# Kernel tuning notes

Hardware: AMD Instinct MI355X
Metric: run time of the kernel (lower is better)

## Reference

```python
import jax, jax.numpy as jnp
import numpy as np

B = 2048          # number of graphs in the batch
ACT_DIM = 14      # nodes per graph (act_dim)
C = 128           # in_channels
H = 256           # hidden_size


def _pair_edges(n):
    ii, jj = np.meshgrid(np.arange(n), np.arange(n), indexing='ij')
    m = ii != jj
    return np.stack([ii[m], jj[m]], axis=1)  # [n*(n-1), 2]


def setup_inputs() -> dict:
    key = jax.random.key(0)
    ks = jax.random.split(key, 12)
    edges_np = _pair_edges(ACT_DIM)                       # [182, 2]
    offs = (np.arange(B) * ACT_DIM)[:, None, None]
    batched = (edges_np[None] + offs).reshape(-1, 2)      # [B*182, 2]
    edge_index = jnp.asarray(batched.T, dtype=jnp.int64 if jax.config.jax_enable_x64 else jnp.int32)
    edges = jnp.asarray(edges_np, dtype=jnp.int32)

    def lin(k, o, i):
        return jax.random.normal(k, (o, i), jnp.float32) * (1.0 / np.sqrt(i))

    return {
        'state': jax.random.normal(ks[0], (B * ACT_DIM, C), jnp.float32),
        'conv_w': lin(ks[1], C, C),
        'conv_b': jnp.zeros((C,), jnp.float32),
        'lin1_w': lin(ks[2], H, 2 * C),
        'lin1_b': jax.random.normal(ks[3], (H,), jnp.float32) * 0.01,
        'lin2_w': lin(ks[4], H, H),
        'lin2_b': jax.random.normal(ks[5], (H,), jnp.float32) * 0.01,
        'mu_w': lin(ks[6], 1, H),
        'mu_b': jnp.zeros((1,), jnp.float32),
        'sig_w': lin(ks[7], 1, H),
        'sig_b': jnp.zeros((1,), jnp.float32),
        'noise': jax.random.normal(ks[8], (B, edges_np.shape[0]), jnp.float32),
        'edge_index': edge_index,
        'edges': edges,
    }


def _gcn_conv(x, edge_index, w, b):
    # Standard GCNConv: add self-loops, symmetric normalization, x @ W^T, scatter-add, + bias.
    n = x.shape[0]
    loops = jnp.arange(n, dtype=edge_index.dtype)
    src = jnp.concatenate([edge_index[0], loops])
    dst = jnp.concatenate([edge_index[1], loops])
    deg = jax.ops.segment_sum(jnp.ones_like(src, dtype=x.dtype), dst, num_segments=n)
    dinv = jax.lax.rsqrt(deg)  # deg >= 1 because of self-loops
    norm = dinv[src] * dinv[dst]                       # [E+N]
    xw = x @ w.T                                       # [N, C]
    msg = xw[src] * norm[:, None]                      # gather + scale
    return jax.ops.segment_sum(msg, dst, num_segments=n) + b


def reference(state, conv_w, conv_b, lin1_w, lin1_b, lin2_w, lin2_b,
              mu_w, mu_b, sig_w, sig_b, noise, edge_index, edges):
    out = jax.nn.relu(_gcn_conv(state, edge_index, conv_w, conv_b))
    x = (out + state).reshape(-1, ACT_DIM, C)          # [B, 14, C]
    es, ed = edges[:, 0], edges[:, 1]
    ef = jnp.concatenate([x[:, es, :], x[:, ed, :]], axis=2)   # [B, E, 2C]
    h = jax.nn.leaky_relu(jnp.einsum('bec,hc->beh', ef, lin1_w) + lin1_b)
    h = jax.nn.leaky_relu(jnp.einsum('beh,gh->beg', h, lin2_w) + lin2_b)
    mu = jax.nn.softplus(jnp.einsum('beh,oh->beo', h, mu_w) + mu_b)[..., 0]   # [B, E]
    std = jax.nn.softplus(jnp.einsum('beh,oh->beo', h, sig_w) + sig_b)[..., 0]
    action = mu + std * noise                          # Normal rsample with fixed eps
    log_prob = jnp.sum(
        -0.5 * ((action - mu) / std) ** 2 - jnp.log(std) - 0.5 * jnp.log(2.0 * jnp.pi),
        axis=-1)                                       # [B]
    return action, log_prob
```

## Files before the change

kernel.cpp:

```cpp
#include <hip/hip_runtime.h>
#include <hip/hip_bf16.h>

#define ACT 14
#define CC 128
#define HH 256
#define EPB 182
#define NB 2048
#define M2 (NB*EPB)
#define NS 520
#define LP_CONST (-182.0f * 0.91893853320467274f)

typedef short s16x8 __attribute__((ext_vector_type(8)));
typedef float f32x4 __attribute__((ext_vector_type(4)));
typedef int   i32x4 __attribute__((ext_vector_type(4)));
typedef float f32x16 __attribute__((ext_vector_type(16)));

__device__ __forceinline__ short f2bf(float f) {
    unsigned u = __float_as_uint(f);
    unsigned r = (u + 0x7fffu + ((u >> 16) & 1u)) >> 16;
    return (short)r;
}
__device__ __forceinline__ float b2f(short s) {
    return __uint_as_float(((unsigned)(unsigned short)s) << 16);
}
__device__ __forceinline__ float bflo(int m) { return __uint_as_float(((unsigned)m) << 16); }
__device__ __forceinline__ float bfhi(int m) { return __uint_as_float((unsigned)m & 0xffff0000u); }
__device__ __forceinline__ float leaky(float x) { return fmaxf(x, 0.01f * x); }
__device__ __forceinline__ float softplusf(float x) { return x > 15.f ? x : log1pf(expf(x)); }

union bf2u { __hip_bfloat162 h; int i; };
__device__ __forceinline__ int pk_bf16(float a, float b) {
    bf2u u; u.h = __float22bfloat162_rn(make_float2(a, b));
    return u.i;
}

__global__ __launch_bounds__(256) void prep_kernel(
    const float* __restrict__ conv_w, const float* __restrict__ lin1_w,
    const float* __restrict__ lin2_w, const float* __restrict__ mu_w,
    const float* __restrict__ sig_w, const float* __restrict__ lin2_b,
    short* __restrict__ W2bf, short* __restrict__ W1bf,
    short* __restrict__ cwbf, short* __restrict__ w1sbf,
    int* __restrict__ msbf, int* __restrict__ b2p)
{
    int i = blockIdx.x * 256 + threadIdx.x;
    W2bf[i] = f2bf(lin2_w[i]);
    {
        int n = i >> 7, k = i & 127;
        float v = (n < 256) ? lin1_w[n * 256 + k] : lin1_w[(n - 256) * 256 + 128 + k];
        W1bf[i] = f2bf(v);
    }
    if (i < 16384) cwbf[i] = f2bf(conv_w[i]);
    if (i < 32768) {
        int h = i >> 7, k = i & 127;
        w1sbf[i] = f2bf(lin1_w[h * 256 + k] + lin1_w[h * 256 + 128 + k]);
    }
    if (i < 256) msbf[i] = pk_bf16(mu_w[i], sig_w[i]);
    if (i < 128) b2p[i] = pk_bf16(lin2_b[2 * i], lin2_b[2 * i + 1]);
}

__global__ __launch_bounds__(512, 4) void actor_kernel(
    const float* __restrict__ state, const short* __restrict__ W1bf,
    const short* __restrict__ W2bf,
    const short* __restrict__ cwbf, const float* __restrict__ conv_b,
    const short* __restrict__ w1sbf, const float* __restrict__ lin1_b,
    const int* __restrict__ b2p, const int* __restrict__ msbf,
    const float* __restrict__ mu_b, const float* __restrict__ sig_b,
    const float* __restrict__ noise, const int* __restrict__ edges,
    float* __restrict__ out)
{
    __shared__ short h1L[8192];
    __shared__ short nodeL[2 * ACT * NS];
    __shared__ float wL[2][256];
    __shared__ int   b2pL[128];
    __shared__ int   msL[256];
    __shared__ float mu_acc[384], sg_acc[384];
    __shared__ float lp_acc[2];

    short* stateL = &h1L[0];
    float* ssumLp = (float*)&h1L[5120];
    float* gLp    = (float*)&h1L[5632];

    const int t = threadIdx.x, b = blockIdx.x;
    const int lane = t & 63, ln = lane & 15, q = lane >> 4;
    const int w = t >> 6;
    const int l32 = lane & 31, hf = lane >> 5;

    #pragma unroll
    for (int it = 0; it < 2; ++it) {
        int idx = it * 512 + t;
        int bt = idx >> 9, row = (idx >> 5) & 15, c4 = idx & 31;
        int kk = c4 >> 3, k8 = (c4 & 7) * 4;
        int* dst = (int*)&stateL[bt * 2560 + kk * 640 + row * 40 + k8];
        if (row < ACT) {
            f32x4 x = *(const f32x4*)(state + ((size_t)(2 * b + bt) * ACT + row) * CC + c4 * 4);
            dst[0] = pk_bf16(x[0], x[1]); dst[1] = pk_bf16(x[2], x[3]);
        } else { dst[0] = 0; dst[1] = 0; }
    }
    if (t < 256) {
        msL[t] = msbf[t];
        if (t < 128) b2pL[t] = b2p[t];
    } else {
        int i = t - 256, bt = i >> 7, c = i & 127;
        const float* sp = state + (size_t)(2 * b + bt) * ACT * CC + c;
        float s = 0.f;
        #pragma unroll
        for (int r = 0; r < ACT; ++r) s += sp[r * CC];
        ssumLp[bt * 128 + c] = s * (1.f / 14.f);
    }
    if (t < 384) { mu_acc[t] = 0.f; sg_acc[t] = 0.f; }
    if (t < 2) lp_acc[t] = 0.f;
    __syncthreads();

    if (t < 256) {
        int bt = t >> 7, j = t & 127;
        const short* cw = cwbf + j * CC;
        const float* ss = ssumLp + bt * 128;
        float a0 = 0.f, a1 = 0.f;
        #pragma unroll
        for (int c8 = 0; c8 < 16; ++c8) {
            s16x8 w8 = *(const s16x8*)(cw + c8 * 8);
            f32x4 s0 = *(const f32x4*)(ss + c8 * 8);
            f32x4 s1 = *(const f32x4*)(ss + c8 * 8 + 4);
            a0 += b2f(w8[0]) * s0[0]; a1 += b2f(w8[1]) * s0[1];
            a0 += b2f(w8[2]) * s0[2]; a1 += b2f(w8[3]) * s0[3];
            a0 += b2f(w8[4]) * s1[0]; a1 += b2f(w8[5]) * s1[1];
            a0 += b2f(w8[6]) * s1[2]; a1 += b2f(w8[7]) * s1[3];
        }
        gLp[bt * 128 + j] = fmaxf(a0 + a1 + conv_b[j], 0.f);
    }
    __syncthreads();
    {
        int bt = t >> 8, h = t & 255;
        const short* ww = w1sbf + h * CC;
        const float* gg = gLp + bt * 128;
        float a0 = 0.f, a1 = 0.f;
        #pragma unroll
        for (int c8 = 0; c8 < 16; ++c8) {
            s16x8 w8 = *(const s16x8*)(ww + c8 * 8);
            f32x4 s0 = *(const f32x4*)(gg + c8 * 8);
            f32x4 s1 = *(const f32x4*)(gg + c8 * 8 + 4);
            a0 += b2f(w8[0]) * s0[0]; a1 += b2f(w8[1]) * s0[1];
            a0 += b2f(w8[2]) * s0[2]; a1 += b2f(w8[3]) * s0[3];
            a0 += b2f(w8[4]) * s1[0]; a1 += b2f(w8[5]) * s1[1];
            a0 += b2f(w8[6]) * s1[2]; a1 += b2f(w8[7]) * s1[3];
        }
        wL[bt][h] = a0 + a1 + lin1_b[h];
    }
    __syncthreads();

    f32x4 zero4 = {0.f, 0.f, 0.f, 0.f};
    f32x4 nacc[2][4];
    #pragma unroll
    for (int bt = 0; bt < 2; ++bt) {
        nacc[bt][0] = zero4; nacc[bt][1] = zero4;
        nacc[bt][2] = zero4; nacc[bt][3] = zero4;
    }
    #pragma unroll
    for (int c = 0; c < 4; ++c) {
        s16x8 a80 = *(const s16x8*)&stateL[0 * 2560 + c * 640 + ln * 40 + q * 8];
        s16x8 a81 = *(const s16x8*)&stateL[1 * 2560 + c * 640 + ln * 40 + q * 8];
        #pragma unroll
        for (int i = 0; i < 4; ++i) {
            int ct = w + 8 * i;
            s16x8 b8 = *(const s16x8*)&W1bf[(size_t)(ct * 16 + ln) * CC + c * 32 + q * 8];
            nacc[0][i] = __builtin_amdgcn_mfma_f32_16x16x32_bf16(a80, b8, nacc[0][i], 0, 0, 0);
            nacc[1][i] = __builtin_amdgcn_mfma_f32_16x16x32_bf16(a81, b8, nacc[1][i], 0, 0, 0);
        }
    }
    #pragma unroll
    for (int bt = 0; bt < 2; ++bt)
        #pragma unroll
        for (int i = 0; i < 4; ++i) {
            int col = (w + 8 * i) * 16 + ln;
            float wadd = (col < HH) ? wL[bt][col] : 0.f;
            #pragma unroll
            for (int rg = 0; rg < 4; ++rg) {
                int node = q * 4 + rg;
                if (node < ACT) nodeL[(bt * ACT + node) * NS + col] = f2bf(nacc[bt][i][rg] + wadd);
            }
        }
    __syncthreads();

    const short* wp = W2bf + (size_t)(w * 32 + l32) * HH + hf * 8;

    auto build = [&](int tile) {
        int bt = (tile >= 6) ? 1 : 0;
        int e32 = t & 31;
        int e = (tile - bt * 6) * 32 + e32;
        bool ok = e < EPB;
        int base = bt * ACT * NS;
        int uo = base, vo = base + HH;
        if (ok) { int2 p = ((const int2*)edges)[e]; uo += p.x * NS; vo += p.y * NS; }
        int sl = t >> 5;
        #pragma unroll
        for (int s = 0; s < 2; ++s) {
            int slot = sl + 16 * s;
            int chunk = slot >> 1, half = slot & 1;
            int koff = chunk * 16 + half * 8;
            int o[4] = {0, 0, 0, 0};
            if (ok) {
                s16x8 u8 = *(const s16x8*)&nodeL[uo + koff];
                s16x8 v8 = *(const s16x8*)&nodeL[vo + koff];
                const int* ui = (const int*)&u8;
                const int* vi = (const int*)&v8;
                #pragma unroll
                for (int j = 0; j < 4; ++j) {
                    int uu = ui[j], vv = vi[j];
                    float s0 = bflo(uu) + bflo(vv);
                    float s1 = bfhi(uu) + bfhi(vv);
                    o[j] = pk_bf16(leaky(s0), leaky(s1));
                }
            }
            *(s16x8*)&h1L[chunk * 512 + (half * 32 + e32) * 8] = *(const s16x8*)o;
        }
    };

    for (int tile = 0; tile < 12; ++tile) {
        build(tile);
        __syncthreads();
        f32x16 acc;
        #pragma unroll
        for (int r = 0; r < 16; ++r) acc[r] = 0.f;
        s16x8 wcur = *(const s16x8*)(wp);
        #pragma unroll
        for (int c = 0; c < 16; ++c) {
            s16x8 wnxt;
            if (c < 15) wnxt = *(const s16x8*)(wp + (c + 1) * 16);
            s16x8 b8 = *(const s16x8*)&h1L[c * 512 + lane * 8];
            acc = __builtin_amdgcn_mfma_f32_32x32x16_bf16(wcur, b8, acc, 0, 0, 0);
            wcur = wnxt;
        }
        int bt = (tile >= 6) ? 1 : 0;
        int col0 = (tile - bt * 6) * 32;
        float pmu = 0.f, psg = 0.f;
        const int nsb = w * 32 + 4 * hf;
        #pragma unroll
        for (int g = 0; g < 4; ++g) {
            int2 bp = *(const int2*)&b2pL[(nsb >> 1) + 4 * g];
            i32x4 m4 = *(const i32x4*)&msL[nsb + 8 * g];
            float h0 = leaky(acc[g * 4 + 0] + bflo(bp.x));
            float h1 = leaky(acc[g * 4 + 1] + bfhi(bp.x));
            float h2 = leaky(acc[g * 4 + 2] + bflo(bp.y));
            float h3 = leaky(acc[g * 4 + 3] + bfhi(bp.y));
            pmu += bflo(m4[0]) * h0 + bflo(m4[1]) * h1 + bflo(m4[2]) * h2 + bflo(m4[3]) * h3;
            psg += bfhi(m4[0]) * h0 + bfhi(m4[1]) * h1 + bfhi(m4[2]) * h2 + bfhi(m4[3]) * h3;
        }
        pmu += __shfl_xor(pmu, 32);
        psg += __shfl_xor(psg, 32);
        if (lane < 32) {
            atomicAdd(&mu_acc[bt * 192 + col0 + l32], pmu);
            atomicAdd(&sg_acc[bt * 192 + col0 + l32], psg);
        }
        __syncthreads();
    }

    float lpv = 0.f;
    {
        int bt = t >> 8, i = t & 255;
        if (i < EPB) {
            float mu = softplusf(mu_acc[bt * 192 + i] + mu_b[0]);
            float sd = softplusf(sg_acc[bt * 192 + i] + sig_b[0]);
            float z = noise[(size_t)(2 * b + bt) * EPB + i];
            out[(size_t)(2 * b + bt) * EPB + i] = mu + sd * z;
            lpv = -0.5f * z * z - logf(sd);
        }
    }
    #pragma unroll
    for (int off = 1; off < 64; off <<= 1) lpv += __shfl_xor(lpv, off);
    if (lane == 0) atomicAdd(&lp_acc[t >> 8], lpv);
    __syncthreads();
    if (t < 2) out[M2 + 2 * b + t] = lp_acc[t] + LP_CONST;
}

extern "C" void kernel_launch(void* const* d_in, const int* in_sizes, int n_in,
                              void* d_out, int out_size, void* d_ws, size_t ws_size,
                              hipStream_t stream)
{
    const float* state  = (const float*)d_in[0];
    const float* conv_w = (const float*)d_in[1];
    const float* conv_b = (const float*)d_in[2];
    const float* lin1_w = (const float*)d_in[3];
    const float* lin1_b = (const float*)d_in[4];
    const float* lin2_w = (const float*)d_in[5];
    const float* lin2_b = (const float*)d_in[6];
    const float* mu_w   = (const float*)d_in[7];
    const float* mu_b   = (const float*)d_in[8];
    const float* sig_w  = (const float*)d_in[9];
    const float* sig_b  = (const float*)d_in[10];
    const float* noise  = (const float*)d_in[11];
    const int*   edges  = (const int*)d_in[13];
    float* out = (float*)d_out;

    char* ws = (char*)d_ws;
    short* W2bf  = (short*)ws;  ws += 65536 * 2;
    short* W1bf  = (short*)ws;  ws += 65536 * 2;
    short* cwbf  = (short*)ws;  ws += 16384 * 2;
    short* w1sbf = (short*)ws;  ws += 32768 * 2;
    int*   msbf  = (int*)ws;    ws += 256 * 4;
    int*   b2p   = (int*)ws;    ws += 128 * 4;

    prep_kernel<<<256, 256, 0, stream>>>(conv_w, lin1_w, lin2_w, mu_w, sig_w, lin2_b,
                                         W2bf, W1bf, cwbf, w1sbf, msbf, b2p);
    actor_kernel<<<NB / 2, 512, 0, stream>>>(state, W1bf, W2bf,
                                             cwbf, conv_b, w1sbf, lin1_b,
                                             b2p, msbf, mu_b, sig_b,
                                             noise, edges, out);
}
```

Baseline: 222.1 us.

## Build edge features in registers per wave and keep lin2 weights resident

Each wave now builds its own MFMA B operand (leaky(u+v) edge features) straight from nodeL into registers, instead of writing a shared h1L tile and synchronising twice per tile. The wave's slice of the lin2 weights is loaded once into 16 registers before the loop rather than reloaded from global memory every tile. This removes the per-tile block barriers and the LDS round trip. In exchange every wave redundantly recomputes the edge features for its tile, up to eight times the old build work, and register pressure rises, which may cut occupancy under launch_bounds(512,4).

```diff
diff --git a/kernel.cpp b/kernel.cpp
--- a/kernel.cpp
+++ b/kernel.cpp
@@ -68,17 +68,15 @@
     const float* __restrict__ noise, const int* __restrict__ edges,
     float* __restrict__ out)
 {
-    __shared__ short h1L[8192];
+    __shared__ short stateL[5120];
     __shared__ short nodeL[2 * ACT * NS];
+    __shared__ float ssumL[256];
+    __shared__ float gLs[256];
     __shared__ float wL[2][256];
     __shared__ int   b2pL[128];
     __shared__ int   msL[256];
     __shared__ float mu_acc[384], sg_acc[384];
     __shared__ float lp_acc[2];
-
-    short* stateL = &h1L[0];
-    float* ssumLp = (float*)&h1L[5120];
-    float* gLp    = (float*)&h1L[5632];
 
     const int t = threadIdx.x, b = blockIdx.x;
     const int lane = t & 63, ln = lane & 15, q = lane >> 4;
@@ -105,7 +103,7 @@
         float s = 0.f;
         #pragma unroll
         for (int r = 0; r < ACT; ++r) s += sp[r * CC];
-        ssumLp[bt * 128 + c] = s * (1.f / 14.f);
+        ssumL[bt * 128 + c] = s * (1.f / 14.f);
     }
     if (t < 384) { mu_acc[t] = 0.f; sg_acc[t] = 0.f; }
     if (t < 2) lp_acc[t] = 0.f;
@@ -114,7 +112,7 @@
     if (t < 256) {
         int bt = t >> 7, j = t & 127;
         const short* cw = cwbf + j * CC;
-        const float* ss = ssumLp + bt * 128;
+        const float* ss = ssumL + bt * 128;
         float a0 = 0.f, a1 = 0.f;
         #pragma unroll
         for (int c8 = 0; c8 < 16; ++c8) {
@@ -126,13 +124,13 @@
             a0 += b2f(w8[4]) * s1[0]; a1 += b2f(w8[5]) * s1[1];
             a0 += b2f(w8[6]) * s1[2]; a1 += b2f(w8[7]) * s1[3];
         }
-        gLp[bt * 128 + j] = fmaxf(a0 + a1 + conv_b[j], 0.f);
+        gLs[bt * 128 + j] = fmaxf(a0 + a1 + conv_b[j], 0.f);
     }
     __syncthreads();
     {
         int bt = t >> 8, h = t & 255;
         const short* ww = w1sbf + h * CC;
-        const float* gg = gLp + bt * 128;
+        const float* gg = gLs + bt * 128;
         float a0 = 0.f, a1 = 0.f;
         #pragma unroll
         for (int c8 = 0; c8 < 16; ++c8) {
@@ -179,58 +177,42 @@
                 if (node < ACT) nodeL[(bt * ACT + node) * NS + col] = f2bf(nacc[bt][i][rg] + wadd);
             }
         }
-    __syncthreads();
-
-    const short* wp = W2bf + (size_t)(w * 32 + l32) * HH + hf * 8;
-
-    auto build = [&](int tile) {
+
+    s16x8 wa[16];
+    #pragma unroll
+    for (int c = 0; c < 16; ++c)
+        wa[c] = *(const s16x8*)&W2bf[(size_t)(w * 32 + l32) * HH + c * 16 + hf * 8];
+    __syncthreads();
+
+    const int koff0 = hf * 8;
+    for (int tile = 0; tile < 12; ++tile) {
         int bt = (tile >= 6) ? 1 : 0;
-        int e32 = t & 31;
-        int e = (tile - bt * 6) * 32 + e32;
-        bool ok = e < EPB;
+        int e = (tile - bt * 6) * 32 + l32;
         int base = bt * ACT * NS;
         int uo = base, vo = base + HH;
-        if (ok) { int2 p = ((const int2*)edges)[e]; uo += p.x * NS; vo += p.y * NS; }
-        int sl = t >> 5;
-        #pragma unroll
-        for (int s = 0; s < 2; ++s) {
-            int slot = sl + 16 * s;
-            int chunk = slot >> 1, half = slot & 1;
-            int koff = chunk * 16 + half * 8;
-            int o[4] = {0, 0, 0, 0};
-            if (ok) {
-                s16x8 u8 = *(const s16x8*)&nodeL[uo + koff];
-                s16x8 v8 = *(const s16x8*)&nodeL[vo + koff];
-                const int* ui = (const int*)&u8;
-                const int* vi = (const int*)&v8;
-                #pragma unroll
-                for (int j = 0; j < 4; ++j) {
-                    int uu = ui[j], vv = vi[j];
-                    float s0 = bflo(uu) + bflo(vv);
-                    float s1 = bfhi(uu) + bfhi(vv);
-                    o[j] = pk_bf16(leaky(s0), leaky(s1));
-                }
+        if (e < EPB) {
+            int2 p = ((const int2*)edges)[e];
+            uo += p.x * NS; vo += p.y * NS;
+        }
+        f32x16 acc;
+        #pragma unroll
+        for (int r = 0; r < 16; ++r) acc[r] = 0.f;
+        #pragma unroll
+        for (int c = 0; c < 16; ++c) {
+            s16x8 u8 = *(const s16x8*)&nodeL[uo + c * 16 + koff0];
+            s16x8 v8 = *(const s16x8*)&nodeL[vo + c * 16 + koff0];
+            const int* ui = (const int*)&u8;
+            const int* vi = (const int*)&v8;
+            int o[4];
+            #pragma unroll
+            for (int j = 0; j < 4; ++j) {
+                int uu = ui[j], vv = vi[j];
+                float s0 = bflo(uu) + bflo(vv);
+                float s1 = bfhi(uu) + bfhi(vv);
+                o[j] = pk_bf16(leaky(s0), leaky(s1));
             }
-            *(s16x8*)&h1L[chunk * 512 + (half * 32 + e32) * 8] = *(const s16x8*)o;
-        }
-    };
-
-    for (int tile = 0; tile < 12; ++tile) {
-        build(tile);
-        __syncthreads();
-        f32x16 acc;
-        #pragma unroll
-        for (int r = 0; r < 16; ++r) acc[r] = 0.f;
-        s16x8 wcur = *(const s16x8*)(wp);
-        #pragma unroll
-        for (int c = 0; c < 16; ++c) {
-            s16x8 wnxt;
-            if (c < 15) wnxt = *(const s16x8*)(wp + (c + 1) * 16);
-            s16x8 b8 = *(const s16x8*)&h1L[c * 512 + lane * 8];
-            acc = __builtin_amdgcn_mfma_f32_32x32x16_bf16(wcur, b8, acc, 0, 0, 0);
-            wcur = wnxt;
-        }
-        int bt = (tile >= 6) ? 1 : 0;
+            acc = __builtin_amdgcn_mfma_f32_32x32x16_bf16(wa[c], *(const s16x8*)o, acc, 0, 0, 0);
+        }
         int col0 = (tile - bt * 6) * 32;
         float pmu = 0.f, psg = 0.f;
         const int nsb = w * 32 + 4 * hf;
@@ -251,8 +233,8 @@
             atomicAdd(&mu_acc[bt * 192 + col0 + l32], pmu);
             atomicAdd(&sg_acc[bt * 192 + col0 + l32], psg);
         }
-        __syncthreads();
-    }
+    }
+    __syncthreads();
 
     float lpv = 0.f;
     {
```

Measured after the change: 312.8 us. 40.8% more time.
